# Performance work log

Measured on AMD Instinct MI355X. Metric: run time of the kernel, lower is better.

The kernel has to match this reference:

```python
import jax, jax.numpy as jnp
import numpy as np

B, T, D, R = 8, 2048, 2048, 4


def setup_inputs() -> dict:
    key = jax.random.key(0)
    ks = jax.random.split(key, 9)
    u = jax.random.normal(ks[0], (B, T, D), dtype=jnp.float32)
    # a chosen so tanh(a) ~ 0.995: keeps cumprod over T=2048 away from underflow
    a = 3.0 + 0.2 * jax.random.uniform(ks[1], (D,), dtype=jnp.float32)
    b = 0.02 * jax.random.normal(ks[2], (D,), dtype=jnp.float32)
    c = 0.02 * jax.random.normal(ks[3], (D,), dtype=jnp.float32)
    d = 0.02 * jax.random.normal(ks[4], (D,), dtype=jnp.float32)
    gate_w = jax.random.normal(ks[5], (D, D), dtype=jnp.float32) / np.float32(np.sqrt(D))
    gate_b = jnp.zeros((D,), dtype=jnp.float32)
    d_lr_u = 0.02 * jax.random.normal(ks[6], (D, R), dtype=jnp.float32)
    d_lr_v = 0.02 * jax.random.normal(ks[7], (R, D), dtype=jnp.float32)
    return {"u": u, "a": a, "b": b, "c": c, "d": d,
            "gate_w": gate_w, "gate_b": gate_b,
            "d_lr_u": d_lr_u, "d_lr_v": d_lr_v}


def reference(u, a, b, c, d, gate_w, gate_b, d_lr_u, d_lr_v):
    # u: [B,T,D]
    Bs, Ts, Ds = u.shape
    rank = d_lr_u.shape[1]
    # gated input (torch Linear: x @ W.T + bias)
    g = jax.nn.sigmoid(jnp.einsum('btd,ed->bte', u, gate_w) + gate_b)
    u_g = u * g
    aa = jnp.tanh(a)                                   # [D], in (-1,1)
    # low-rank correction to feedthrough d
    u_mean = jnp.mean(u_g, axis=1, keepdims=True)      # [B,1,D]
    d_lr = (u_mean @ d_lr_u) @ d_lr_v / max(1.0, float(rank))
    d_eff = d + d_lr                                   # [B,1,D]
    # diagonal SSM via cumprod/cumsum (G[t] = aa^(t+1)); per-channel, T-independent of B
    G = jnp.cumprod(jnp.broadcast_to(aa, (Ts, Ds)), axis=0)  # [T,D]
    bu = b * u_g                                       # [B,T,D]
    G_safe = G.at[0].set(jnp.maximum(G[0], 1e-6))
    z = bu / G_safe                                    # [B,T,D]
    s = G * jnp.cumsum(z, axis=1)                      # [B,T,D]
    y = c * s + d_eff * u_g
    return y
```

## Files before the change

### kernel.cpp

```cpp
#include <hip/hip_runtime.h>
#include <hip/hip_bf16.h>
#include <math.h>

#define Bq 8
#define Tq 2048
#define Dq 2048
#define Rq 4
#define Mq (Bq*Tq)
#define NC 16
#define CL (Tq/NC)

typedef __attribute__((ext_vector_type(8))) short bf16x8;
typedef __attribute__((ext_vector_type(4))) float f32x4;
typedef __attribute__((ext_vector_type(4))) unsigned short us4;
typedef __attribute__((ext_vector_type(8))) unsigned short us8;

__device__ __forceinline__ unsigned short f2bf(float x) {
    unsigned int u = __float_as_uint(x);
    unsigned int r = (u + 0x7fffu + ((u >> 16) & 1u)) >> 16;
    return (unsigned short)r;
}
__device__ __forceinline__ float bf2f(unsigned short h) {
    return __uint_as_float((unsigned)h << 16);
}

template<int UGBF>
__device__ __forceinline__ f32x4 ld4(const void* p, long long off) {
    if constexpr (UGBF) {
        us4 v = *(const us4*)((const unsigned short*)p + off);
        f32x4 r;
        r.x = bf2f(v.x); r.y = bf2f(v.y); r.z = bf2f(v.z); r.w = bf2f(v.w);
        return r;
    } else {
        return *(const f32x4*)((const float*)p + off);
    }
}

__global__ __launch_bounds__(256) void k0_convert(
    const float* __restrict__ u, const float* __restrict__ gw,
    const float* __restrict__ a,
    unsigned short* __restrict__ ubf, unsigned short* __restrict__ wbf,
    float* __restrict__ aat, float* __restrict__ aaLt,
    float* __restrict__ aapow)
{
    const long long uN4 = (long long)Mq * Dq / 4;
    const long long wN4 = (long long)Dq * Dq / 4;
    long long gid = (long long)blockIdx.x * blockDim.x + threadIdx.x;
    if (gid < Dq) {
        float aa = tanhf(a[gid]);
        aat[gid] = aa;
        aaLt[gid] = exp2f((float)CL * log2f(aa));
        float p = 1.0f;
        for (int k = 0; k <= 16; ++k) { aapow[k * Dq + gid] = p; p *= aa; }
    }
    long long stride = (long long)gridDim.x * blockDim.x;
    for (long long i = gid; i < uN4 + wN4; i += stride) {
        const float4* src; unsigned short* dst; long long j;
        if (i < uN4) { src = (const float4*)u;  dst = ubf; j = i; }
        else         { src = (const float4*)gw; dst = wbf; j = i - uN4; }
        float4 v = src[j];
        us4 p;
        p.x = f2bf(v.x); p.y = f2bf(v.y); p.z = f2bf(v.z); p.w = f2bf(v.w);
        *(us4*)(dst + j * 4) = p;
    }
}


#define PH_BAR __builtin_amdgcn_s_barrier()
#define PRIO1  __builtin_amdgcn_s_setprio(1)
#define PRIO0  __builtin_amdgcn_s_setprio(0)

#define LDA(K0, K1, qb) do { _Pragma("unroll") for (int f_ = 0; f_ < 4; ++f_) { \
    aF[0][f_] = *(const bf16x8*)&lds[(K0) + ((qb) + f_) * 1024]; \
    aF[1][f_] = *(const bf16x8*)&lds[(K1) + ((qb) + f_) * 1024]; } } while (0)

#define LDB(K0, K1, fnb) do { _Pragma("unroll") for (int f_ = 0; f_ < 2; ++f_) { \
    bF[0][(fnb) + f_] = *(const bf16x8*)&lds[(K0) + ((fnb) + f_) * 1024]; \
    bF[1][(fnb) + f_] = *(const bf16x8*)&lds[(K1) + ((fnb) + f_) * 1024]; } } while (0)

#define MMA(fmb, fnb) do { _Pragma("unroll") for (int ks_ = 0; ks_ < 2; ++ks_) \
    _Pragma("unroll") for (int fm_ = 0; fm_ < 4; ++fm_) \
    _Pragma("unroll") for (int fn_ = 0; fn_ < 2; ++fn_) \
        acc[(fmb) + fm_][(fnb) + fn_] = __builtin_amdgcn_mfma_f32_16x16x32_bf16( \
            aF[ks_][fm_], bF[ks_][(fnb) + fn_], acc[(fmb) + fm_][(fnb) + fn_], 0, 0, 0); } while (0)

#define GLD(P, DST) __builtin_amdgcn_global_load_lds( \
    (const __attribute__((address_space(1))) void*)(P), \
    (__attribute__((address_space(3))) void*)&lds[DST], 16, 0, 0)

#define STAGE2(P0, P1, DBASE, KOFF) do { \
    GLD((P0) + (KOFF), (DBASE));         \
    GLD((P1) + (KOFF), (DBASE) + 512); } while (0)

template<int UGBF>
__global__ __launch_bounds__(512, 2) void k1_gemm(
    const unsigned short* __restrict__ Abf,
    const unsigned short* __restrict__ Bbf,
    const float* __restrict__ gate_b,
    const float* __restrict__ bvec,
    const float* __restrict__ aapow,
    float* __restrict__ psum,
    float* __restrict__ carry,
    void* __restrict__ ug_)
{
    __shared__ unsigned short lds[65536];
    const int tid  = threadIdx.x;
    const int wave = tid >> 6, lane = tid & 63;
    const int wr = wave >> 2, wc = wave & 3;

    const int bid = blockIdx.x;
    const int swz = (bid & 7) * 64 + (bid >> 3);
    const int tm = (swz >> 3) * 256;
    const int tn = (swz & 7) * 256;

    const int rr = lane & 15, kq = lane >> 4;
    const int r7 = rr & 7;
    const int kb0 = (kq ^ r7) * 8;
    const int kb1 = ((4 + kq) ^ r7) * 8;

    const int aB = wr * 8192 + rr * 64;
    const int bB = 16384 + (wc >> 1) * 8192 + (wc & 1) * 4096 + rr * 64;
    const int swA0k0 = aB + kb0,          swA0k1 = aB + kb1;
    const int swA1k0 = aB + 32768 + kb0,  swA1k1 = aB + 32768 + kb1;
    const int swB0k0 = bB + kb0,          swB0k1 = bB + kb1;
    const int swB1k0 = bB + 32768 + kb0,  swB1k1 = bB + 32768 + kb1;

    const int grow  = lane >> 3;
    const int gslot = ((lane & 7) ^ grow) * 8;
    const unsigned short* gA00 = Abf + (long long)(tm + wave * 16 + grow) * Dq + gslot;
    const unsigned short* gA01 = gA00 + 8 * Dq;
    const unsigned short* gA10 = gA00 + 128 * Dq;
    const unsigned short* gA11 = gA00 + 136 * Dq;
    const unsigned short* gB00 = Bbf + (long long)(tn + wave * 16 + grow) * Dq + gslot;
    const unsigned short* gB01 = gB00 + 8 * Dq;
    const unsigned short* gB10 = gB00 + 128 * Dq;
    const unsigned short* gB11 = gB00 + 136 * Dq;

    f32x4 acc[8][4] = {};
    bf16x8 aF[2][4], bF[2][4];

    const int dA0 = wave * 1024;
    const int dB0 = 16384 + wave * 1024;

    STAGE2(gA00, gA01, dA0,                0);
    STAGE2(gA10, gA11, dA0 + 8192,         0);
    STAGE2(gB00, gB01, dB0,                0);
    STAGE2(gB10, gB11, dB0 + 8192,         0);
    STAGE2(gB00, gB01, dB0 + 32768,        64);
    STAGE2(gB10, gB11, dB0 + 32768 + 8192, 64);
    asm volatile("s_waitcnt vmcnt(4)" ::: "memory");
    PH_BAR;

    const int NIT = Dq / 128;
    for (int it = 0; it < NIT; ++it) {
        const bool pre = (it < NIT - 1);

        LDA(swA0k0, swA0k1, 0); LDB(swB0k0, swB0k1, 0);
        STAGE2(gA00, gA01, dA0 + 32768, 64);
        asm volatile("s_waitcnt lgkmcnt(8)" ::: "memory");
        PH_BAR; PRIO1; MMA(0, 0); PRIO0; PH_BAR;

        LDB(swB0k0, swB0k1, 2);
        STAGE2(gA10, gA11, dA0 + 32768 + 8192, 64);
        PH_BAR; PRIO1; MMA(0, 2); PRIO0; PH_BAR;

        LDA(swA0k0, swA0k1, 4);
        if (pre) STAGE2(gB00, gB01, dB0, 128);
        PH_BAR; PRIO1; MMA(4, 0); PRIO0; PH_BAR;

        if (pre) {
            STAGE2(gB10, gB11, dB0 + 8192, 128);
            asm volatile("s_waitcnt vmcnt(4)" ::: "memory");
        } else {
            asm volatile("s_waitcnt vmcnt(0)" ::: "memory");
        }
        PH_BAR; PRIO1; MMA(4, 2); PRIO0; PH_BAR;

        LDA(swA1k0, swA1k1, 0); LDB(swB1k0, swB1k1, 0);
        if (pre) STAGE2(gA00, gA01, dA0, 128);
        asm volatile("s_waitcnt lgkmcnt(8)" ::: "memory");
        PH_BAR; PRIO1; MMA(0, 0); PRIO0; PH_BAR;

        LDB(swB1k0, swB1k1, 2);
        if (pre) STAGE2(gA10, gA11, dA0 + 8192, 128);
        PH_BAR; PRIO1; MMA(0, 2); PRIO0; PH_BAR;

        LDA(swA1k0, swA1k1, 4);
        if (pre) STAGE2(gB00, gB01, dB0 + 32768, 192);
        PH_BAR; PRIO1; MMA(4, 0); PRIO0; PH_BAR;

        if (pre) {
            STAGE2(gB10, gB11, dB0 + 32768 + 8192, 192);
            asm volatile("s_waitcnt vmcnt(4)" ::: "memory");
        }
        PH_BAR; PRIO1; MMA(4, 2); PRIO0; PH_BAR;

        gA00 += 128; gA01 += 128; gA10 += 128; gA11 += 128;
        gB00 += 128; gB01 += 128; gB10 += 128; gB11 += 128;
    }

#pragma unroll
    for (int fn = 0; fn < 4; ++fn) {
        const int col = wc * 64 + fn * 16 + rr;
        const float gb = gate_b[tn + col];
#pragma unroll
        for (int fm = 0; fm < 8; ++fm) {
#pragma unroll
            for (int j = 0; j < 4; ++j) {
                const int row = wr * 128 + fm * 16 + kq * 4 + j;
                const float logit = acc[fm][fn][j] + gb;
                const float sg = 1.0f / (1.0f + __expf(-logit));
                lds[row * 256 + (col ^ (kq << 4))] = f2bf(sg);
            }
        }
    }
    __syncthreads();

    const int lr2  = lane >> 5;
    const int cb32 = lane & 31;
    const int c0   = cb32 * 8;
    const int baseT = wave * 2 + lr2;
    const int cX = ((baseT >> 2) & 3) << 4;

    float bw[8], a16[8], w15[8];
    {
        const float* bp   = bvec + tn + c0;
        const float* a16p = aapow + 16 * Dq + tn + c0;
        const float* w15p = aapow + (15 - baseT) * Dq + tn + c0;
#pragma unroll
        for (int k = 0; k < 8; ++k) { bw[k] = bp[k]; a16[k] = a16p[k]; w15[k] = w15p[k]; }
    }

    float ps[2][8] = {}, cr[2][8] = {};
#pragma unroll
    for (int i = 0; i < 16; ++i) {
        const int r = baseT + i * 16;
        const int ck = i >> 3;
        const long long gidx = (long long)(tm + r) * Dq + tn + c0;
        const bf16x8 u8 = *(const bf16x8*)&Abf[gidx];
        const bf16x8 s8 = *(const bf16x8*)&lds[r * 256 + (c0 ^ cX)];
        float ug[8];
#pragma unroll
        for (int k = 0; k < 8; ++k) {
            ug[k] = bf2f((unsigned short)u8[k]) * bf2f((unsigned short)s8[k]);
            ps[ck][k] += ug[k];
            cr[ck][k] = a16[k] * cr[ck][k] + bw[k] * ug[k];
        }
        if constexpr (UGBF) {
            us8 o;
#pragma unroll
            for (int k = 0; k < 8; ++k) o[k] = f2bf(ug[k]);
            *(us8*)&((unsigned short*)ug_)[gidx] = o;
        } else {
            f32x4 o0, o1;
            o0.x = ug[0]; o0.y = ug[1]; o0.z = ug[2]; o0.w = ug[3];
            o1.x = ug[4]; o1.y = ug[5]; o1.z = ug[6]; o1.w = ug[7];
            *(f32x4*)&((float*)ug_)[gidx]     = o0;
            *(f32x4*)&((float*)ug_)[gidx + 4] = o1;
        }
    }
    __syncthreads();

    float* redf = (float*)lds;
    const int slot = (baseT + cb32) & 15;
#pragma unroll
    for (int ck = 0; ck < 2; ++ck)
#pragma unroll
        for (int k = 0; k < 8; ++k) {
            const int col = c0 + k;
            redf[((ck * 2 + 0) * 256 + col) * 16 + slot] = ps[ck][k];
            redf[((ck * 2 + 1) * 256 + col) * 16 + slot] = cr[ck][k] * w15[k];
        }
    __syncthreads();

    const int bb  = tm >> 11;
    const int ckb = (tm & 2047) >> 7;
#pragma unroll
    for (int ii = 0; ii < 2; ++ii) {
        const int item = tid + ii * 512;
        const int p = item >> 8, col = item & 255;
        const int ck = p >> 1, isC = p & 1;
        const int rot = (item & 3) * 4;
        float s = 0.f;
#pragma unroll
        for (int q = 0; q < 4; ++q) {
            const f32x4 v = *(const f32x4*)&redf[item * 16 + ((rot + q * 4) & 15)];
            s += v.x + v.y + v.z + v.w;
        }
        const long long gi = (long long)(bb * NC + ckb + ck) * Dq + tn + col;
        if (isC) carry[gi] = s; else psum[gi] = s;
    }
}

__global__ __launch_bounds__(256) void k3_deff(
    const float* __restrict__ psum, const float* __restrict__ dvec,
    const float* __restrict__ dlru, const float* __restrict__ dlrv,
    float* __restrict__ deff)
{
    const int bb = blockIdx.x, tid = threadIdx.x;
    __shared__ float red[4][256];
    __shared__ float proj[4];
    float pr[4] = {0.f, 0.f, 0.f, 0.f};
    for (int i = 0; i < Dq / 256; ++i) {
        int dd = tid + i * 256;
        float m = 0.f;
        for (int k = 0; k < NC; ++k) m += psum[((long long)bb * NC + k) * Dq + dd];
        m *= (1.0f / (float)Tq);
#pragma unroll
        for (int r = 0; r < 4; ++r) pr[r] += m * dlru[dd * Rq + r];
    }
#pragma unroll
    for (int r = 0; r < 4; ++r) red[r][tid] = pr[r];
    __syncthreads();
    for (int off = 128; off > 0; off >>= 1) {
        if (tid < off)
#pragma unroll
            for (int r = 0; r < 4; ++r) red[r][tid] += red[r][tid + off];
        __syncthreads();
    }
    if (tid < 4) proj[tid] = red[tid][0] * 0.25f;
    __syncthreads();
    float p0 = proj[0], p1 = proj[1], p2 = proj[2], p3 = proj[3];
    for (int i = 0; i < Dq / 256; ++i) {
        int e = tid + i * 256;
        float v = dvec[e] + p0 * dlrv[0 * Dq + e] + p1 * dlrv[1 * Dq + e]
                          + p2 * dlrv[2 * Dq + e] + p3 * dlrv[3 * Dq + e];
        deff[(long long)bb * Dq + e] = v;
    }
}

template<int UGBF>
__global__ __launch_bounds__(128) void k4_scanC(
    const void* __restrict__ ug, float* __restrict__ yout,
    const float* __restrict__ aat, const float* __restrict__ aaLt,
    const float* __restrict__ bvec, const float* __restrict__ cvec,
    const float* __restrict__ deff, const float* __restrict__ carry)
{
    const int d0 = blockIdx.x * 512 + threadIdx.x * 4;
    const int ck = blockIdx.y, bb = blockIdx.z;
    f32x4 aa  = *(const f32x4*)&aat[d0];
    f32x4 aaL = *(const f32x4*)&aaLt[d0];
    f32x4 bv  = *(const f32x4*)&bvec[d0];
    f32x4 cv  = *(const f32x4*)&cvec[d0];
    f32x4 de  = *(const f32x4*)&deff[(long long)bb * Dq + d0];
    f32x4 s = {0.f, 0.f, 0.f, 0.f};
    for (int j = 0; j < ck; ++j) {
        f32x4 cj = *(const f32x4*)&carry[((long long)bb * NC + j) * Dq + d0];
        s = aaL * s + cj;
    }
    const long long base = ((long long)bb * Tq + (long long)ck * CL) * Dq + d0;
    for (int t = 0; t < CL; ++t) {
        f32x4 x = ld4<UGBF>(ug, base + (long long)t * Dq);
        s = aa * s + bv * x;
        f32x4 y = cv * s + de * x;
        *(f32x4*)&yout[base + (long long)t * Dq] = y;
    }
}

extern "C" void kernel_launch(void* const* d_in, const int* in_sizes, int n_in,
                              void* d_out, int out_size, void* d_ws, size_t ws_size,
                              hipStream_t stream)
{
    const float* u    = (const float*)d_in[0];
    const float* a    = (const float*)d_in[1];
    const float* b    = (const float*)d_in[2];
    const float* c    = (const float*)d_in[3];
    const float* d    = (const float*)d_in[4];
    const float* gw   = (const float*)d_in[5];
    const float* gb   = (const float*)d_in[6];
    const float* dlru = (const float*)d_in[7];
    const float* dlrv = (const float*)d_in[8];
    float* out = (float*)d_out;

    char* ws = (char*)d_ws;
    const size_t sz_ubf = (size_t)Mq * Dq * 2;
    const size_t sz_wbf = (size_t)Dq * Dq * 2;
    const size_t sz_ug  = (size_t)Mq * Dq * 2;
    const size_t sz_ps  = (size_t)Bq * NC * Dq * 4;

    unsigned short* ubf = (unsigned short*)ws;
    unsigned short* wbf = (unsigned short*)(ws + sz_ubf);

    const size_t tail_sz = 2 * sz_ps + (size_t)Bq * Dq * 4
                         + 2 * (size_t)Dq * 4 + (size_t)17 * Dq * 4;
    const size_t need_bf16 = sz_ubf + sz_wbf + sz_ug + tail_sz;
    const bool ugbf_mode = (ws_size >= need_bf16);

    char* rest = ws + sz_ubf + sz_wbf;
    unsigned short* ugbf = (unsigned short*)rest;
    char* tail = ugbf_mode ? (rest + sz_ug) : rest;
    float* psum  = (float*)tail;
    float* carry = psum  + (size_t)Bq * NC * Dq;
    float* deff  = carry + (size_t)Bq * NC * Dq;
    float* aat   = deff  + (size_t)Bq * Dq;
    float* aaLt  = aat   + Dq;
    float* aapow = aaLt  + Dq;

    k0_convert<<<2048, 256, 0, stream>>>(u, gw, a, ubf, wbf, aat, aaLt, aapow);

    dim3 g2(Dq / 512, NC, Bq);
    if (ugbf_mode) {
        k1_gemm<1><<<512, 512, 0, stream>>>(ubf, wbf, gb, b, aapow, psum, carry, ugbf);
        k3_deff<<<Bq, 256, 0, stream>>>(psum, d, dlru, dlrv, deff);
        k4_scanC<1><<<g2, 128, 0, stream>>>(ugbf, out, aat, aaLt, b, c, deff, carry);
    } else {
        k1_gemm<0><<<512, 512, 0, stream>>>(ubf, wbf, gb, b, aapow, psum, carry, out);
        k3_deff<<<Bq, 256, 0, stream>>>(psum, d, dlru, dlrv, deff);
        k4_scanC<0><<<g2, 128, 0, stream>>>(out, out, aat, aaLt, b, c, deff, carry);
    }
}
```

Measured before the change: 234.3 us.

## Fuse fp32-to-bf16 conversion of u into GEMM A-tile loading

Drops the separate pass that converted u (128 MB fp32) to bf16. The GEMM now loads fp32 u through registers, converts to bf16 and writes it into swizzled LDS in place of the direct global-to-LDS loads, and the epilogue reads fp32 u directly. This removes a full read-write pass over u. In exchange the main loop gains register pressure, VALU conversion work and twice the A-tile global traffic.

```diff
diff --git a/kernel.cpp b/kernel.cpp
--- a/kernel.cpp
+++ b/kernel.cpp
@@ -37,13 +37,11 @@
 }
 
 __global__ __launch_bounds__(256) void k0_convert(
-    const float* __restrict__ u, const float* __restrict__ gw,
-    const float* __restrict__ a,
-    unsigned short* __restrict__ ubf, unsigned short* __restrict__ wbf,
+    const float* __restrict__ gw, const float* __restrict__ a,
+    unsigned short* __restrict__ wbf,
     float* __restrict__ aat, float* __restrict__ aaLt,
     float* __restrict__ aapow)
 {
-    const long long uN4 = (long long)Mq * Dq / 4;
     const long long wN4 = (long long)Dq * Dq / 4;
     long long gid = (long long)blockIdx.x * blockDim.x + threadIdx.x;
     if (gid < Dq) {
@@ -54,14 +52,11 @@
         for (int k = 0; k <= 16; ++k) { aapow[k * Dq + gid] = p; p *= aa; }
     }
     long long stride = (long long)gridDim.x * blockDim.x;
-    for (long long i = gid; i < uN4 + wN4; i += stride) {
-        const float4* src; unsigned short* dst; long long j;
-        if (i < uN4) { src = (const float4*)u;  dst = ubf; j = i; }
-        else         { src = (const float4*)gw; dst = wbf; j = i - uN4; }
-        float4 v = src[j];
+    for (long long j = gid; j < wN4; j += stride) {
+        float4 v = ((const float4*)gw)[j];
         us4 p;
         p.x = f2bf(v.x); p.y = f2bf(v.y); p.z = f2bf(v.z); p.w = f2bf(v.w);
-        *(us4*)(dst + j * 4) = p;
+        *(us4*)(wbf + j * 4) = p;
     }
 }
 
@@ -92,9 +87,24 @@
     GLD((P0) + (KOFF), (DBASE));         \
     GLD((P1) + (KOFF), (DBASE) + 512); } while (0)
 
+#define AISSUE(R, P, KOFF) do { const float* p_ = (P) + (KOFF); \
+    R[0] = *(const f32x4*)(p_);     R[1] = *(const f32x4*)(p_ + 4); \
+    R[2] = *(const f32x4*)(p_ + 8); R[3] = *(const f32x4*)(p_ + 12); } while (0)
+
+#define ACOMMIT(DBASE) do { us8 w0_, w1_, w2_, w3_; \
+    _Pragma("unroll") for (int q_ = 0; q_ < 4; ++q_) { \
+        w0_[q_] = f2bf(sA0[0][q_]); w0_[4 + q_] = f2bf(sA0[1][q_]); \
+        w1_[q_] = f2bf(sA0[2][q_]); w1_[4 + q_] = f2bf(sA0[3][q_]); \
+        w2_[q_] = f2bf(sA1[0][q_]); w2_[4 + q_] = f2bf(sA1[1][q_]); \
+        w3_[q_] = f2bf(sA1[2][q_]); w3_[4 + q_] = f2bf(sA1[3][q_]); } \
+    *(us8*)&lds[(DBASE) + arow * 64 + as0]        = w0_; \
+    *(us8*)&lds[(DBASE) + arow * 64 + as1]        = w1_; \
+    *(us8*)&lds[(DBASE) + 8192 + arow * 64 + as0] = w2_; \
+    *(us8*)&lds[(DBASE) + 8192 + arow * 64 + as1] = w3_; } while (0)
+
 template<int UGBF>
 __global__ __launch_bounds__(512, 2) void k1_gemm(
-    const unsigned short* __restrict__ Abf,
+    const float* __restrict__ uf,
     const unsigned short* __restrict__ Bbf,
     const float* __restrict__ gate_b,
     const float* __restrict__ bvec,
@@ -127,28 +137,34 @@
 
     const int grow  = lane >> 3;
     const int gslot = ((lane & 7) ^ grow) * 8;
-    const unsigned short* gA00 = Abf + (long long)(tm + wave * 16 + grow) * Dq + gslot;
-    const unsigned short* gA01 = gA00 + 8 * Dq;
-    const unsigned short* gA10 = gA00 + 128 * Dq;
-    const unsigned short* gA11 = gA00 + 136 * Dq;
     const unsigned short* gB00 = Bbf + (long long)(tn + wave * 16 + grow) * Dq + gslot;
     const unsigned short* gB01 = gB00 + 8 * Dq;
     const unsigned short* gB10 = gB00 + 128 * Dq;
     const unsigned short* gB11 = gB00 + 136 * Dq;
 
+    const int arow = tid >> 2;
+    const int aj   = tid & 3;
+    const int ar7  = arow & 7;
+    const int as0  = (((aj << 1))     ^ ar7) * 8;
+    const int as1  = (((aj << 1) | 1) ^ ar7) * 8;
+    const float* gAh0 = uf + (long long)(tm + arow) * Dq + aj * 16;
+    const float* gAh1 = gAh0 + 128 * Dq;
+
     f32x4 acc[8][4] = {};
     bf16x8 aF[2][4], bF[2][4];
-
-    const int dA0 = wave * 1024;
+    f32x4 sA0[4], sA1[4];
+
     const int dB0 = 16384 + wave * 1024;
 
-    STAGE2(gA00, gA01, dA0,                0);
-    STAGE2(gA10, gA11, dA0 + 8192,         0);
-    STAGE2(gB00, gB01, dB0,                0);
-    STAGE2(gB10, gB11, dB0 + 8192,         0);
-    STAGE2(gB00, gB01, dB0 + 32768,        64);
+    AISSUE(sA0, gAh0, 0); AISSUE(sA1, gAh1, 0);
+    STAGE2(gB00, gB01, dB0, 0); STAGE2(gB10, gB11, dB0 + 8192, 0);
+    asm volatile("s_waitcnt vmcnt(4)" ::: "memory");
+    ACOMMIT(0);
+    AISSUE(sA0, gAh0, 64); AISSUE(sA1, gAh1, 64);
+    STAGE2(gB00, gB01, dB0 + 32768, 64);
     STAGE2(gB10, gB11, dB0 + 32768 + 8192, 64);
     asm volatile("s_waitcnt vmcnt(4)" ::: "memory");
+    ACOMMIT(32768);
     PH_BAR;
 
     const int NIT = Dq / 128;
@@ -156,12 +172,12 @@
         const bool pre = (it < NIT - 1);
 
         LDA(swA0k0, swA0k1, 0); LDB(swB0k0, swB0k1, 0);
-        STAGE2(gA00, gA01, dA0 + 32768, 64);
+        if (pre) AISSUE(sA0, gAh0, 128);
         asm volatile("s_waitcnt lgkmcnt(8)" ::: "memory");
         PH_BAR; PRIO1; MMA(0, 0); PRIO0; PH_BAR;
 
         LDB(swB0k0, swB0k1, 2);
-        STAGE2(gA10, gA11, dA0 + 32768 + 8192, 64);
+        if (pre) AISSUE(sA1, gAh1, 128);
         PH_BAR; PRIO1; MMA(0, 2); PRIO0; PH_BAR;
 
         LDA(swA0k0, swA0k1, 4);
@@ -171,18 +187,19 @@
         if (pre) {
             STAGE2(gB10, gB11, dB0 + 8192, 128);
             asm volatile("s_waitcnt vmcnt(4)" ::: "memory");
+            ACOMMIT(0);
         } else {
             asm volatile("s_waitcnt vmcnt(0)" ::: "memory");
         }
         PH_BAR; PRIO1; MMA(4, 2); PRIO0; PH_BAR;
 
         LDA(swA1k0, swA1k1, 0); LDB(swB1k0, swB1k1, 0);
-        if (pre) STAGE2(gA00, gA01, dA0, 128);
+        if (pre) AISSUE(sA0, gAh0, 192);
         asm volatile("s_waitcnt lgkmcnt(8)" ::: "memory");
         PH_BAR; PRIO1; MMA(0, 0); PRIO0; PH_BAR;
 
         LDB(swB1k0, swB1k1, 2);
-        if (pre) STAGE2(gA10, gA11, dA0 + 8192, 128);
+        if (pre) AISSUE(sA1, gAh1, 192);
         PH_BAR; PRIO1; MMA(0, 2); PRIO0; PH_BAR;
 
         LDA(swA1k0, swA1k1, 4);
@@ -192,10 +209,11 @@
         if (pre) {
             STAGE2(gB10, gB11, dB0 + 32768 + 8192, 192);
             asm volatile("s_waitcnt vmcnt(4)" ::: "memory");
+            ACOMMIT(32768);
         }
         PH_BAR; PRIO1; MMA(4, 2); PRIO0; PH_BAR;
 
-        gA00 += 128; gA01 += 128; gA10 += 128; gA11 += 128;
+        gAh0 += 128; gAh1 += 128;
         gB00 += 128; gB01 += 128; gB10 += 128; gB11 += 128;
     }
 
@@ -237,12 +255,14 @@
         const int r = baseT + i * 16;
         const int ck = i >> 3;
         const long long gidx = (long long)(tm + r) * Dq + tn + c0;
-        const bf16x8 u8 = *(const bf16x8*)&Abf[gidx];
+        const f32x4 ua = *(const f32x4*)&uf[gidx];
+        const f32x4 ub = *(const f32x4*)&uf[gidx + 4];
         const bf16x8 s8 = *(const bf16x8*)&lds[r * 256 + (c0 ^ cX)];
+        float uk[8] = {ua.x, ua.y, ua.z, ua.w, ub.x, ub.y, ub.z, ub.w};
         float ug[8];
 #pragma unroll
         for (int k = 0; k < 8; ++k) {
-            ug[k] = bf2f((unsigned short)u8[k]) * bf2f((unsigned short)s8[k]);
+            ug[k] = uk[k] * bf2f((unsigned short)s8[k]);
             ps[ck][k] += ug[k];
             cr[ck][k] = a16[k] * cr[ck][k] + bw[k] * ug[k];
         }
@@ -373,20 +393,18 @@
     float* out = (float*)d_out;
 
     char* ws = (char*)d_ws;
-    const size_t sz_ubf = (size_t)Mq * Dq * 2;
     const size_t sz_wbf = (size_t)Dq * Dq * 2;
     const size_t sz_ug  = (size_t)Mq * Dq * 2;
     const size_t sz_ps  = (size_t)Bq * NC * Dq * 4;
 
-    unsigned short* ubf = (unsigned short*)ws;
-    unsigned short* wbf = (unsigned short*)(ws + sz_ubf);
+    unsigned short* wbf = (unsigned short*)ws;
 
     const size_t tail_sz = 2 * sz_ps + (size_t)Bq * Dq * 4
                          + 2 * (size_t)Dq * 4 + (size_t)17 * Dq * 4;
-    const size_t need_bf16 = sz_ubf + sz_wbf + sz_ug + tail_sz;
+    const size_t need_bf16 = sz_wbf + sz_ug + tail_sz;
     const bool ugbf_mode = (ws_size >= need_bf16);
 
-    char* rest = ws + sz_ubf + sz_wbf;
+    char* rest = ws + sz_wbf;
     unsigned short* ugbf = (unsigned short*)rest;
     char* tail = ugbf_mode ? (rest + sz_ug) : rest;
     float* psum  = (float*)tail;
@@ -396,15 +414,15 @@
     float* aaLt  = aat   + Dq;
     float* aapow = aaLt  + Dq;
 
-    k0_convert<<<2048, 256, 0, stream>>>(u, gw, a, ubf, wbf, aat, aaLt, aapow);
+    k0_convert<<<512, 256, 0, stream>>>(gw, a, wbf, aat, aaLt, aapow);
 
     dim3 g2(Dq / 512, NC, Bq);
     if (ugbf_mode) {
-        k1_gemm<1><<<512, 512, 0, stream>>>(ubf, wbf, gb, b, aapow, psum, carry, ugbf);
+        k1_gemm<1><<<512, 512, 0, stream>>>(u, wbf, gb, b, aapow, psum, carry, ugbf);
         k3_deff<<<Bq, 256, 0, stream>>>(psum, d, dlru, dlrv, deff);
         k4_scanC<1><<<g2, 128, 0, stream>>>(ugbf, out, aat, aaLt, b, c, deff, carry);
     } else {
-        k1_gemm<0><<<512, 512, 0, stream>>>(ubf, wbf, gb, b, aapow, psum, carry, out);
+        k1_gemm<0><<<512, 512, 0, stream>>>(u, wbf, gb, b, aapow, psum, carry, out);
         k3_deff<<<Bq, 256, 0, stream>>>(psum, d, dlru, dlrv, deff);
         k4_scanC<0><<<g2, 128, 0, stream>>>(out, out, aat, aaLt, b, c, deff, carry);
     }
```

Measured after the change: 274.1 us. 1.17x slower.
